# Kernel tuning notes

Hardware: AMD Instinct MI355X
Metric: run time of the kernel (lower is better)

## Reference

```python
import jax, jax.numpy as jnp
import numpy as np
from jax import lax

EPS = 1e-5  # flax BatchNorm default epsilon

def _conv(x, k, b):
    y = lax.conv_general_dilated(x, k, (1, 1), 'SAME', dimension_numbers=('NHWC', 'HWIO', 'NHWC'))
    return y + b

def _bn(x, s, o, m, v):
    # BatchNorm with use_running_average=True (eval mode)
    return (x - m) * (s / jnp.sqrt(v + EPS)) + o

def _pool(x):
    return lax.reduce_window(x, -jnp.inf, lax.max, (1, 2, 2, 1), (1, 2, 2, 1), 'SAME')

def _lstm_last(x_seq, Wi, Wh, b):
    # x_seq: [T,B,D]; Wi: [L,D,4H]; Wh: [L,H,4H]; b: [L,4H].
    # Faithful to original bug: every layer consumes the SAME raw input x_seq
    # (layers are not stacked); only the last layer's hidden states are used.
    B = x_seq.shape[1]
    H = Wh.shape[1]
    def run_layer(Wi_l, Wh_l, b_l):
        def step(carry, xt):
            h, c = carry
            z = xt @ Wi_l + h @ Wh_l + b_l  # [B,4H]
            i, f, g, o = jnp.split(z, 4, axis=-1)
            c2 = jax.nn.sigmoid(f) * c + jax.nn.sigmoid(i) * jnp.tanh(g)
            h2 = jax.nn.sigmoid(o) * jnp.tanh(c2)
            return (h2, c2), h2
        init = (jnp.zeros((B, H), x_seq.dtype), jnp.zeros((B, H), x_seq.dtype))
        _, hs = lax.scan(step, init, x_seq)
        return hs  # [T,B,H]
    hs_all = jax.vmap(run_layer)(Wi, Wh, b)  # [L,T,B,H]
    return hs_all[-1]


def setup_inputs():
    key = jax.random.key(0)
    ks = iter(jax.random.split(key, 64))
    def nrm(shape, scale=0.05):
        return jax.random.normal(next(ks), shape, jnp.float32) * scale
    d = {}
    d['x'] = jax.random.normal(next(ks), (64, 32, 256, 1), jnp.float32)
    cin = [1, 64, 128, 256, 256]
    cout = [64, 128, 256, 256, 512]
    for i in range(5):
        d[f'k{i+1}'] = nrm((3, 3, cin[i], cout[i]))
        d[f'b{i+1}'] = nrm((cout[i],))
        d[f's{i+1}'] = 1.0 + nrm((cout[i],), 0.1)
        d[f'o{i+1}'] = nrm((cout[i],), 0.1)
        d[f'm{i+1}'] = jnp.zeros((cout[i],), jnp.float32)
        d[f'v{i+1}'] = jnp.ones((cout[i],), jnp.float32)
    L, D, H = 2, 2048, 512
    for pre in ('fw', 'bw'):
        d[f'{pre}_Wi'] = nrm((L, D, 4 * H), 0.02)
        d[f'{pre}_Wh'] = nrm((L, H, 4 * H), 0.02)
        d[f'{pre}_b'] = nrm((L, 4 * H), 0.02)
    d['fc_W'] = nrm((2 * H, 80), 0.02)
    d['fc_b'] = nrm((80,), 0.02)
    return d


def reference(x, k1, b1, k2, b2, k3, b3, k4, b4, k5, b5,
              s1, o1, m1, v1, s2, o2, m2, v2, s3, o3, m3, v3,
              s4, o4, m4, v4, s5, o5, m5, v5,
              fw_Wi, fw_Wh, fw_b, bw_Wi, bw_Wh, bw_b, fc_W, fc_b):
    # CNN stem (eval mode: dropout is identity, BN uses running stats)
    x = _pool(_bn(jax.nn.relu(_conv(x, k1, b1)), s1, o1, m1, v1))
    x = _pool(_bn(jax.nn.relu(_conv(x, k2, b2)), s2, o2, m2, v2))
    x = _pool(_bn(jax.nn.relu(_conv(x, k3, b3)), s3, o3, m3, v3))
    x = _bn(jax.nn.relu(_conv(x, k4, b4)), s4, o4, m4, v4)
    x = _bn(jax.nn.relu(_conv(x, k5, b5)), s5, o5, m5, v5)
    b, h, w, c = x.shape
    x = x.reshape(b, w, h * c)        # faithful raw reshape (no transpose), as in original
    x_seq = jnp.swapaxes(x, 0, 1)     # [T,B,D]
    fw = _lstm_last(x_seq, fw_Wi, fw_Wh, fw_b)          # [T,B,H]
    bw = _lstm_last(x_seq[::-1], bw_Wi, bw_Wh, bw_b)    # [T,B,H]; NOT re-flipped (matches original)
    out = jnp.swapaxes(jnp.concatenate([fw, bw], axis=-1), 0, 1)  # [B,T,2H]
    logits = out @ fc_W + fc_b
    return jax.nn.log_softmax(logits, axis=-1)
```

## Files before the change

kernel.cpp:

```cpp
#include <hip/hip_runtime.h>
#include <hip/hip_bf16.h>
#include <math.h>

#define EPSBN 1e-5f

using short8 = __attribute__((ext_vector_type(8))) short;
using f32x4  = __attribute__((ext_vector_type(4))) float;
using us4    = __attribute__((ext_vector_type(4))) unsigned short;

#define MFMA16(a, b, c) __builtin_amdgcn_mfma_f32_16x16x32_bf16(a, b, c, 0, 0, 0)

__device__ __forceinline__ float bf2f(unsigned short u) {
  unsigned int v = ((unsigned int)u) << 16;
  float f;
  __builtin_memcpy(&f, &v, 4);
  return f;
}
__device__ __forceinline__ unsigned short f2bf(float f) {
  __hip_bfloat16 h = __float2bfloat16(f);
  unsigned short u;
  __builtin_memcpy(&u, &h, 2);
  return u;
}
__device__ __forceinline__ float fast_sigmoid(float z) {
  return __builtin_amdgcn_rcpf(1.f + __expf(-z));
}
__device__ __forceinline__ float fast_tanh(float z) {
  float x2 = fminf(fmaxf(2.f * z, -30.f), 30.f);
  float e = __expf(x2);
  return (e - 1.f) * __builtin_amdgcn_rcpf(e + 1.f);
}
__device__ __forceinline__ void stage16(const unsigned short* g, unsigned short* l) {
  __builtin_amdgcn_global_load_lds(
      (const __attribute__((address_space(1))) void*)g,
      (__attribute__((address_space(3))) void*)l, 16, 0, 0);
}

__global__ __launch_bounds__(256) void conv1_pool(
    const float* __restrict__ in, const float* __restrict__ w,
    const float* __restrict__ bias, const float* __restrict__ sc,
    const float* __restrict__ of, const float* __restrict__ mn,
    const float* __restrict__ vr, unsigned short* __restrict__ out) {
  __shared__ float lds[4][258];
  const int blk = blockIdx.x;
  const int b = blk >> 4, y0 = blk & 15;
  const int tid = threadIdx.x;
  for (int i = tid; i < 4 * 258; i += 256) {
    int row = i / 258, c = i - row * 258;
    int iy = 2 * y0 - 1 + row, xx = c - 1;
    float v = 0.f;
    if ((unsigned)iy < 32u && (unsigned)xx < 256u)
      v = in[((b << 5) + iy) * 256 + xx];
    lds[row][c] = v;
  }
  __syncthreads();
  const int co = tid & 63, xg = tid >> 6;
  float w9[9];
  #pragma unroll
  for (int t = 0; t < 9; ++t) w9[t] = w[t * 64 + co];
  const float scale = sc[co] * rsqrtf(vr[co] + EPSBN);
  const float shift = of[co] - mn[co] * scale;
  const float bs = bias[co];
  unsigned short* op = out + (((long)(b * 18 + y0 + 1) * 130 + xg * 32 + 1) << 6) + co;
  for (int px = 0; px < 32; ++px) {
    const int xp = xg * 32 + px;
    float m = -1e30f;
    #pragma unroll
    for (int dy = 0; dy < 2; ++dy) {
      #pragma unroll
      for (int dx = 0; dx < 2; ++dx) {
        const int x = 2 * xp + dx;
        float acc = bs;
        #pragma unroll
        for (int r = 0; r < 3; ++r)
          #pragma unroll
          for (int cc = 0; cc < 3; ++cc)
            acc = fmaf(lds[dy + r][x + cc], w9[r * 3 + cc], acc);
        float v = fmaxf(acc, 0.f) * scale + shift;
        m = fmaxf(m, v);
      }
    }
    op[(long)px << 6] = f2bf(m);
  }
}

template<int C, int H2, int W2>
__global__ __launch_bounds__(256) void maxpool_pad(
    const unsigned short* __restrict__ in, unsigned short* __restrict__ out) {
  constexpr int W2P = W2 + 2, H2P = H2 + 2;
  const int y = blockIdx.y;
  const int b = y / H2P, yp = y - b * H2P;
  const int j = blockIdx.x * 256 + threadIdx.x;
  if (j >= W2P * C) return;
  const int xp = j / C, c = j - xp * C;
  unsigned short res = 0;
  if (yp >= 1 && yp <= H2 && xp >= 1 && xp <= W2) {
    const long rs = (long)(2 * W2) * C;
    const unsigned short* p0 =
        in + (((long)b * (2 * H2) + (yp - 1) * 2) * (2 * W2) + (xp - 1) * 2) * C + c;
    unsigned short u0 = p0[0], u1 = p0[C], u2 = p0[rs], u3 = p0[rs + C];
    unsigned short a = (bf2f(u0) >= bf2f(u1)) ? u0 : u1;
    unsigned short bmx = (bf2f(u2) >= bf2f(u3)) ? u2 : u3;
    res = (bf2f(a) >= bf2f(bmx)) ? a : bmx;
  }
  out[((long)y * W2P + xp) * C + c] = res;
}

struct TAll {
  const float* src[8];
  unsigned short* dst[8];
  int K[8];
  int N[8];
};
__global__ __launch_bounds__(256) void transpose_multi(TAll P) {
  const int z = blockIdx.z;
  const int K = P.K[z], N = P.N[z];
  const int k0 = blockIdx.x * 32, n0 = blockIdx.y * 32;
  if (k0 >= K || n0 >= N) return;
  __shared__ float T[32][33];
  const float* in = P.src[z];
  unsigned short* out = P.dst[z];
  const int tid = threadIdx.x;
  const int r = tid >> 3, c4 = (tid & 7) * 4;
  float4 v = *(const float4*)(in + (long)(k0 + r) * N + n0 + c4);
  T[r][c4 + 0] = v.x; T[r][c4 + 1] = v.y; T[r][c4 + 2] = v.z; T[r][c4 + 3] = v.w;
  __syncthreads();
  us4 o;
  #pragma unroll
  for (int i = 0; i < 4; ++i) o[i] = f2bf(T[c4 + i][r]);
  *(us4*)(out + (long)(n0 + r) * K + k0 + c4) = o;
}

__global__ __launch_bounds__(256) void transpose_fc(
    const float* __restrict__ W, unsigned short* __restrict__ WT) {
  int i = blockIdx.x * 256 + threadIdx.x;
  if (i < 80 * 1024) {
    int n = i >> 10, k = i & 1023;
    WT[i] = f2bf(W[k * 80 + n]);
  }
}

__global__ __launch_bounds__(256) void zero_multi(
    float* p0, long n0, float* p1, long n1, float* p2, long n2, float* p3, long n3) {
  const long i0 = (long)blockIdx.x * 256 + threadIdx.x;
  const long st = (long)gridDim.x * 256;
  for (long j = i0; j < n0; j += st) p0[j] = 0.f;
  for (long j = i0; j < n1; j += st) p1[j] = 0.f;
  for (long j = i0; j < n2; j += st) p2[j] = 0.f;
  for (long j = i0; j < n3; j += st) p3[j] = 0.f;
}

template<int CIN, int COUT, int H, int W, int OUTPAD>
__global__ __launch_bounds__(256) void conv_mfma128(
    const unsigned short* __restrict__ act, const unsigned short* __restrict__ wT,
    const float* __restrict__ bias, const float* __restrict__ sc,
    const float* __restrict__ of, const float* __restrict__ mn,
    const float* __restrict__ vr, unsigned short* __restrict__ out) {
  constexpr int K9 = 9 * CIN;
  constexpr int HW = H * W;
  constexpr int WP = W + 2;
  constexpr int NK = K9 / 32;
  constexpr int CSH = (CIN == 64) ? 1 : (CIN == 128) ? 2 : 3;
  constexpr int CMSK = (1 << CSH) - 1;
  __shared__ unsigned short As[2][4096];
  __shared__ unsigned short Bs[2][4096];
  const int tid = threadIdx.x;
  const int lane = tid & 63, wave = tid >> 6;
  const int m0 = blockIdx.x * 128, n0 = blockIdx.y * 128;
  const int r0 = tid >> 2, seg = tid & 3;
  const int segp = (seg ^ (r0 & 3)) << 3;
  long pa0, pa1;
  {
    const int m = m0 + r0;
    const int b = m / HW, rem = m % HW;
    const int y = rem / W, x = rem % W;
    pa0 = (((long)b * (H + 2) + y) * WP + x) * CIN + segp;
  }
  {
    const int m = m0 + r0 + 64;
    const int b = m / HW, rem = m % HW;
    const int y = rem / W, x = rem % W;
    pa1 = (((long)b * (H + 2) + y) * WP + x) * CIN + segp;
  }
  const long pb0 = (long)(n0 + r0) * K9 + segp;
  const long pb1 = (long)(n0 + r0 + 64) * K9 + segp;
  const int swz = ((lane >> 4) ^ (lane & 3)) << 3;
  const int arow0 = (wave >> 1) * 64 + (lane & 15);
  const int brow0 = (wave & 1) * 64 + (lane & 15);
  f32x4 acc[4][4] = {};

  auto stage_tile = [&](int ks, int buf) {
    const int tap = ks >> CSH;
    const int cib = (ks & CMSK) << 5;
    const int ty = (tap * 86) >> 8;
    const int tx = tap - ty * 3;
    const long ka = (long)(ty * WP + tx) * CIN + cib;
    const long kb = (long)ks << 5;
    unsigned short* aw = &As[buf][wave * 512];
    unsigned short* bw = &Bs[buf][wave * 512];
    stage16(act + pa0 + ka, aw);
    stage16(act + pa1 + ka, aw + 2048);
    stage16(wT + pb0 + kb, bw);
    stage16(wT + pb1 + kb, bw + 2048);
  };

  stage_tile(0, 0);
  #pragma unroll 1
  for (int ks = 0; ks < NK; ++ks) {
    const int buf = ks & 1;
    if (ks + 1 < NK) {
      stage_tile(ks + 1, buf ^ 1);
      asm volatile("s_waitcnt vmcnt(4)" ::: "memory");
    } else {
      asm volatile("s_waitcnt vmcnt(0)" ::: "memory");
    }
    __builtin_amdgcn_s_barrier();
    __builtin_amdgcn_sched_barrier(0);
    short8 a[4], b[4];
    #pragma unroll
    for (int i = 0; i < 4; ++i)
      a[i] = *(const short8*)(&As[buf][(arow0 + i * 16) * 32 + swz]);
    #pragma unroll
    for (int j = 0; j < 4; ++j)
      b[j] = *(const short8*)(&Bs[buf][(brow0 + j * 16) * 32 + swz]);
    #pragma unroll
    for (int i = 0; i < 4; ++i)
      #pragma unroll
      for (int j = 0; j < 4; ++j)
        acc[i][j] = MFMA16(a[i], b[j], acc[i][j]);
    __builtin_amdgcn_s_barrier();
    __builtin_amdgcn_sched_barrier(0);
  }

  float scl[4], shf[4], bsv[4];
  #pragma unroll
  for (int j = 0; j < 4; ++j) {
    const int col = n0 + (wave & 1) * 64 + j * 16 + (lane & 15);
    scl[j] = sc[col] * rsqrtf(vr[col] + EPSBN);
    shf[j] = of[col] - mn[col] * scl[j];
    bsv[j] = bias[col];
  }
  #pragma unroll
  for (int i = 0; i < 4; ++i) {
    #pragma unroll
    for (int rr = 0; rr < 4; ++rr) {
      const int m = m0 + (wave >> 1) * 64 + i * 16 + (lane >> 4) * 4 + rr;
      const int b = m / HW, rem = m % HW;
      const int y = rem / W, x = rem % W;
      long obase;
      if (OUTPAD) obase = (((long)b * (H + 2) + y + 1) * WP + x + 1) * COUT;
      else        obase = (((long)b * H + y) * W + x) * COUT;
      const int colb = n0 + (wave & 1) * 64 + (lane & 15);
      #pragma unroll
      for (int j = 0; j < 4; ++j) {
        const float v = fmaxf(acc[i][j][rr] + bsv[j], 0.f) * scl[j] + shf[j];
        out[obase + colb + j * 16] = f2bf(v);
      }
    }
  }
}

__global__ __launch_bounds__(256) void gemm_xw128(
    const unsigned short* __restrict__ src, const unsigned short* __restrict__ WiT,
    const float* __restrict__ bvec, float* __restrict__ xw, int rev) {
  __shared__ unsigned short As[2][4096];
  __shared__ unsigned short Bs[2][4096];
  const int tid = threadIdx.x;
  const int lane = tid & 63, wave = tid >> 6;
  const int m0 = blockIdx.x * 128, n0 = blockIdx.y * 128;
  const int r0 = tid >> 2, seg = tid & 3;
  const int segp = (seg ^ (r0 & 3)) << 3;
  long pa0, pa1;
  {
    const int r = m0 + r0;
    const int t = r >> 6, bb = r & 63;
    const int tt = rev ? 31 - t : t;
    pa0 = (long)bb * 65536 + (long)tt * 2048 + segp;
  }
  {
    const int r = m0 + r0 + 64;
    const int t = r >> 6, bb = r & 63;
    const int tt = rev ? 31 - t : t;
    pa1 = (long)bb * 65536 + (long)tt * 2048 + segp;
  }
  const long pb0 = (long)(n0 + r0) * 2048 + segp;
  const long pb1 = (long)(n0 + r0 + 64) * 2048 + segp;
  const int swz = ((lane >> 4) ^ (lane & 3)) << 3;
  const int arow0 = (wave >> 1) * 64 + (lane & 15);
  const int brow0 = (wave & 1) * 64 + (lane & 15);
  f32x4 acc[4][4] = {};

  auto stage_tile = [&](int ks, int buf) {
    const long k0 = (long)ks << 5;
    unsigned short* aw = &As[buf][wave * 512];
    unsigned short* bw = &Bs[buf][wave * 512];
    stage16(src + pa0 + k0, aw);
    stage16(src + pa1 + k0, aw + 2048);
    stage16(WiT + pb0 + k0, bw);
    stage16(WiT + pb1 + k0, bw + 2048);
  };

  stage_tile(0, 0);
  #pragma unroll 1
  for (int ks = 0; ks < 64; ++ks) {
    const int buf = ks & 1;
    if (ks + 1 < 64) {
      stage_tile(ks + 1, buf ^ 1);
      asm volatile("s_waitcnt vmcnt(4)" ::: "memory");
    } else {
      asm volatile("s_waitcnt vmcnt(0)" ::: "memory");
    }
    __builtin_amdgcn_s_barrier();
    __builtin_amdgcn_sched_barrier(0);
    short8 a[4], b[4];
    #pragma unroll
    for (int i = 0; i < 4; ++i)
      a[i] = *(const short8*)(&As[buf][(arow0 + i * 16) * 32 + swz]);
    #pragma unroll
    for (int j = 0; j < 4; ++j)
      b[j] = *(const short8*)(&Bs[buf][(brow0 + j * 16) * 32 + swz]);
    #pragma unroll
    for (int i = 0; i < 4; ++i)
      #pragma unroll
      for (int j = 0; j < 4; ++j)
        acc[i][j] = MFMA16(a[i], b[j], acc[i][j]);
    __builtin_amdgcn_s_barrier();
    __builtin_amdgcn_sched_barrier(0);
  }

  float bsv[4];
  #pragma unroll
  for (int j = 0; j < 4; ++j)
    bsv[j] = bvec[n0 + (wave & 1) * 64 + j * 16 + (lane & 15)];
  #pragma unroll
  for (int i = 0; i < 4; ++i) {
    #pragma unroll
    for (int rr = 0; rr < 4; ++rr) {
      const int row = m0 + (wave >> 1) * 64 + i * 16 + (lane >> 4) * 4 + rr;
      const int colb = n0 + (wave & 1) * 64 + (lane & 15);
      #pragma unroll
      for (int j = 0; j < 4; ++j)
        xw[(long)row * 2048 + colb + j * 16] = acc[i][j][rr] + bsv[j];
    }
  }
}

__global__ __launch_bounds__(256) void lstm_persist(
    const unsigned short* __restrict__ WhTF, const unsigned short* __restrict__ WhTB,
    const float* __restrict__ xwF, const float* __restrict__ xwB,
    unsigned short* __restrict__ hsF, unsigned short* __restrict__ hsB,
    int* __restrict__ bar) {
  __shared__ unsigned short Whs[64 * 512];
  __shared__ unsigned short Hs[64 * 512];
  __shared__ float Zs[4 * 64 * 16];
  const int bid = blockIdx.x;
  const int dir = bid >> 5;
  const int nb = bid & 31;
  const int u0 = nb * 16;
  const unsigned short* WhT = dir ? WhTB : WhTF;
  const float* xw = dir ? xwB : xwF;
  unsigned short* hs = dir ? hsB : hsF;
  int* flagbase = bar + dir * 32 * 16;
  int* myflag = flagbase + nb * 16;
  const int tid = threadIdx.x;
  const int lane = tid & 63, wave = tid >> 6;
  const int lr = lane & 15, lk = lane >> 4;
  const int mp = wave >> 1, gp = wave & 1;

  #pragma unroll
  for (int i = 0; i < 16; ++i) {
    const int G = i * 256 + tid;
    const int row = G >> 6, g8 = G & 63;
    const int g = row >> 4, u = row & 15;
    short8 v = *(const short8*)(WhT + ((long)(g * 512 + u0 + u) << 9) + g8 * 8);
    *(short8*)(Whs + row * 512 + ((g8 ^ (row & 7)) << 3)) = v;
  }

  const int prow = tid >> 2;
  const int pu4 = (tid & 3) * 4;
  float c4[4] = {0.f, 0.f, 0.f, 0.f};
  float4 xq[4];
  #pragma unroll
  for (int g = 0; g < 4; ++g)
    xq[g] = *(const float4*)(xw + (long)prow * 2048 + g * 512 + u0 + pu4);

  for (int t = 0; t < 32; ++t) {
    const unsigned short* hsrc = hs + (long)t * 32768;
    #pragma unroll
    for (int i = 0; i < 16; ++i) {
      const int G = i * 256 + tid;
      const int row = G >> 6, g8 = G & 63;
      short8 v = *(const short8*)(hsrc + G * 8);
      *(short8*)(Hs + row * 512 + ((g8 ^ (row & 7)) << 3)) = v;
    }
    __syncthreads();

    f32x4 acc[2][2] = {};
    #pragma unroll
    for (int kk = 0; kk < 16; ++kk) {
      const int sw = ((lk + kk * 4) ^ (lr & 7)) << 3;
      short8 a0 = *(const short8*)(Hs + (mp * 32 + lr) * 512 + sw);
      short8 a1 = *(const short8*)(Hs + (mp * 32 + 16 + lr) * 512 + sw);
      short8 b0 = *(const short8*)(Whs + (gp * 32 + lr) * 512 + sw);
      short8 b1 = *(const short8*)(Whs + (gp * 32 + 16 + lr) * 512 + sw);
      acc[0][0] = MFMA16(a0, b0, acc[0][0]);
      acc[0][1] = MFMA16(a0, b1, acc[0][1]);
      acc[1][0] = MFMA16(a1, b0, acc[1][0]);
      acc[1][1] = MFMA16(a1, b1, acc[1][1]);
    }

    #pragma unroll
    for (int im = 0; im < 2; ++im) {
      const int rowb = (mp * 2 + im) * 16 + lk * 4;
      #pragma unroll
      for (int ig = 0; ig < 2; ++ig) {
        const int g = gp * 2 + ig;
        #pragma unroll
        for (int r = 0; r < 4; ++r)
          Zs[g * 1024 + (rowb + r) * 16 + lr] = acc[im][ig][r];
      }
    }
    __syncthreads();

    {
      float4 zi = *(const float4*)(Zs + tid * 4);
      float4 zf = *(const float4*)(Zs + 1024 + tid * 4);
      float4 zg = *(const float4*)(Zs + 2048 + tid * 4);
      float4 zo = *(const float4*)(Zs + 3072 + tid * 4);
      const float* pzi = (const float*)&zi;
      const float* pzf = (const float*)&zf;
      const float* pzg = (const float*)&zg;
      const float* pzo = (const float*)&zo;
      us4 hv;
      #pragma unroll
      for (int r = 0; r < 4; ++r) {
        float ii = fast_sigmoid(pzi[r] + ((const float*)&xq[0])[r]);
        float ff = fast_sigmoid(pzf[r] + ((const float*)&xq[1])[r]);
        float gg = fast_tanh(pzg[r] + ((const float*)&xq[2])[r]);
        float oo = fast_sigmoid(pzo[r] + ((const float*)&xq[3])[r]);
        c4[r] = ff * c4[r] + ii * gg;
        hv[r] = f2bf(oo * fast_tanh(c4[r]));
      }
      *(us4*)(hs + (long)(t + 1) * 32768 + prow * 512 + u0 + pu4) = hv;
    }

    if (t < 31) {
      float4 xqn[4];
      #pragma unroll
      for (int g = 0; g < 4; ++g)
        xqn[g] = *(const float4*)(xw + (long)((t + 1) * 64 + prow) * 2048 + g * 512 + u0 + pu4);
      __syncthreads();
      if (tid < 64) {
        if (tid == 0)
          __hip_atomic_store(myflag, t + 1, __ATOMIC_RELEASE, __HIP_MEMORY_SCOPE_AGENT);
        int v;
        do {
          v = __hip_atomic_load(flagbase + (tid & 31) * 16,
                                __ATOMIC_ACQUIRE, __HIP_MEMORY_SCOPE_AGENT);
        } while (__any(v < t + 1));
      }
      __syncthreads();
      #pragma unroll
      for (int g = 0; g < 4; ++g) xq[g] = xqn[g];
    }
  }
}

__global__ __launch_bounds__(256) void fc_mfma_ls(
    const unsigned short* __restrict__ hsF, const unsigned short* __restrict__ hsB,
    const unsigned short* __restrict__ WT, const float* __restrict__ bias,
    float* __restrict__ out) {
  __shared__ unsigned short As_[128 * 32];
  __shared__ unsigned short Bs_[80 * 32];
  __shared__ float zbuf[128][81];
  __shared__ float rmax[128];
  __shared__ float rlse[128];
  const int tid = threadIdx.x;
  const int lane = tid & 63, wave = tid >> 6;
  const int m0 = blockIdx.x * 128;
  const int r0 = tid >> 2, seg = tid & 3;
  const int segp = (seg ^ (r0 & 3)) << 3;
  const int swz = ((lane >> 4) ^ (lane & 3)) << 3;
  f32x4 acc[2][5] = {};

  int bA0, tA0, bA1, tA1;
  { int r = m0 + r0;      bA0 = r >> 5; tA0 = r & 31; }
  { int r = m0 + r0 + 64; bA1 = r >> 5; tA1 = r & 31; }

  #pragma unroll 1
  for (int k0 = 0; k0 < 1024; k0 += 32) {
    const unsigned short* src = (k0 < 512) ? hsF : hsB;
    const int koff = k0 & 511;
    stage16(src + (long)(tA0 + 1) * 32768 + bA0 * 512 + koff + segp, As_ + wave * 512);
    stage16(src + (long)(tA1 + 1) * 32768 + bA1 * 512 + koff + segp, As_ + wave * 512 + 2048);
    {
      int G = tid;
      #pragma unroll
      for (int it = 0; it < 2; ++it, G += 256) {
        int rn = G >> 2, sg = G & 3;
        if (rn < 80) {
          short8 v = *(const short8*)(WT + (long)rn * 1024 + k0 + sg * 8);
          *(short8*)(Bs_ + rn * 32 + ((sg ^ (rn & 3)) << 3)) = v;
        }
      }
    }
    __syncthreads();
    short8 a[2], bfrag[5];
    #pragma unroll
    for (int i = 0; i < 2; ++i)
      a[i] = *(const short8*)(As_ + (wave * 32 + i * 16 + (lane & 15)) * 32 + swz);
    #pragma unroll
    for (int j = 0; j < 5; ++j)
      bfrag[j] = *(const short8*)(Bs_ + (j * 16 + (lane & 15)) * 32 + swz);
    #pragma unroll
    for (int i = 0; i < 2; ++i)
      #pragma unroll
      for (int j = 0; j < 5; ++j)
        acc[i][j] = MFMA16(a[i], bfrag[j], acc[i][j]);
    __syncthreads();
  }

  float bsv[5];
  #pragma unroll
  for (int j = 0; j < 5; ++j) bsv[j] = bias[j * 16 + (lane & 15)];
  #pragma unroll
  for (int i = 0; i < 2; ++i)
    #pragma unroll
    for (int j = 0; j < 5; ++j)
      #pragma unroll
      for (int rr = 0; rr < 4; ++rr)
        zbuf[wave * 32 + i * 16 + (lane >> 4) * 4 + rr][j * 16 + (lane & 15)] =
            acc[i][j][rr] + bsv[j];
  __syncthreads();

  if (tid < 128) {
    float mx = -1e30f;
    for (int j = 0; j < 80; ++j) mx = fmaxf(mx, zbuf[tid][j]);
    float s = 0.f;
    for (int j = 0; j < 80; ++j) s += __expf(zbuf[tid][j] - mx);
    rmax[tid] = mx;
    rlse[tid] = logf(s);
  }
  __syncthreads();

  for (int idx = tid; idx < 128 * 80; idx += 256) {
    const int row = idx / 80, j = idx - row * 80;
    out[(long)m0 * 80 + idx] = zbuf[row][j] - rmax[row] - rlse[row];
  }
}

extern "C" void kernel_launch(void* const* d_in, const int* in_sizes, int n_in,
                              void* d_out, int out_size, void* d_ws, size_t ws_size,
                              hipStream_t stream) {
  const float* x  = (const float*)d_in[0];
  const float* k1 = (const float*)d_in[1];  const float* b1 = (const float*)d_in[2];
  const float* s1 = (const float*)d_in[3];  const float* o1 = (const float*)d_in[4];
  const float* m1 = (const float*)d_in[5];  const float* v1 = (const float*)d_in[6];
  const float* k2 = (const float*)d_in[7];  const float* b2 = (const float*)d_in[8];
  const float* s2 = (const float*)d_in[9];  const float* o2 = (const float*)d_in[10];
  const float* m2 = (const float*)d_in[11]; const float* v2 = (const float*)d_in[12];
  const float* k3 = (const float*)d_in[13]; const float* b3 = (const float*)d_in[14];
  const float* s3 = (const float*)d_in[15]; const float* o3 = (const float*)d_in[16];
  const float* m3 = (const float*)d_in[17]; const float* v3 = (const float*)d_in[18];
  const float* k4 = (const float*)d_in[19]; const float* b4 = (const float*)d_in[20];
  const float* s4 = (const float*)d_in[21]; const float* o4 = (const float*)d_in[22];
  const float* m4 = (const float*)d_in[23]; const float* v4 = (const float*)d_in[24];
  const float* k5 = (const float*)d_in[25]; const float* b5 = (const float*)d_in[26];
  const float* s5 = (const float*)d_in[27]; const float* o5 = (const float*)d_in[28];
  const float* m5 = (const float*)d_in[29]; const float* v5 = (const float*)d_in[30];
  const float* fwWi = (const float*)d_in[31];
  const float* fwWh = (const float*)d_in[32];
  const float* fwb  = (const float*)d_in[33];
  const float* bwWi = (const float*)d_in[34];
  const float* bwWh = (const float*)d_in[35];
  const float* bwb  = (const float*)d_in[36];
  const float* fcW  = (const float*)d_in[37];
  const float* fcb  = (const float*)d_in[38];

  char* wsb = (char*)d_ws;
  unsigned short* REG_A = (unsigned short*)(wsb);
  unsigned short* REG_P = (unsigned short*)(wsb + 33554432);
  unsigned short* C4    = (unsigned short*)(wsb + 52723712);
  unsigned short* wT2   = (unsigned short*)(wsb + 59408384);
  unsigned short* wT3   = (unsigned short*)(wsb + 59555840);
  unsigned short* wT4   = (unsigned short*)(wsb + 60145664);
  unsigned short* wT5   = (unsigned short*)(wsb + 61325312);
  unsigned short* WiTF  = (unsigned short*)(wsb + 63684608);
  unsigned short* WiTB  = (unsigned short*)(wsb + 72073216);
  unsigned short* WhTF  = (unsigned short*)(wsb + 80461824);
  unsigned short* WhTB  = (unsigned short*)(wsb + 82558976);
  unsigned short* WTfc  = (unsigned short*)(wsb + 84656128);
  float* xwF = (float*)(wsb + 84819968);
  float* xwB = (float*)(wsb + 101597184);
  int*   bar = (int*)(wsb + 118374400);
  unsigned short* hsF = (unsigned short*)(wsb + 118378496);
  unsigned short* hsB = (unsigned short*)(wsb + 120541184);

  zero_multi<<<2048, 256, 0, stream>>>(
      (float*)(wsb + 118374400), 17408,
      (float*)(wsb + 120541184), 16384,
      (float*)(wsb + 52723712), 1671168,
      (float*)(wsb + 33554432), 4792320);

  TAll tp;
  tp.src[0] = k2; tp.dst[0] = wT2; tp.K[0] = 576;  tp.N[0] = 128;
  tp.src[1] = k3; tp.dst[1] = wT3; tp.K[1] = 1152; tp.N[1] = 256;
  tp.src[2] = k4; tp.dst[2] = wT4; tp.K[2] = 2304; tp.N[2] = 256;
  tp.src[3] = k5; tp.dst[3] = wT5; tp.K[3] = 2304; tp.N[3] = 512;
  tp.src[4] = fwWi + 4194304; tp.dst[4] = WiTF; tp.K[4] = 2048; tp.N[4] = 2048;
  tp.src[5] = bwWi + 4194304; tp.dst[5] = WiTB; tp.K[5] = 2048; tp.N[5] = 2048;
  tp.src[6] = fwWh + 1048576; tp.dst[6] = WhTF; tp.K[6] = 512;  tp.N[6] = 2048;
  tp.src[7] = bwWh + 1048576; tp.dst[7] = WhTB; tp.K[7] = 512;  tp.N[7] = 2048;
  transpose_multi<<<dim3(72, 64, 8), 256, 0, stream>>>(tp);
  transpose_fc<<<320, 256, 0, stream>>>(fcW, WTfc);

  conv1_pool<<<1024, 256, 0, stream>>>(x, k1, b1, s1, o1, m1, v1, REG_P);

  conv_mfma128<64, 128, 16, 128, 0><<<dim3(1024, 1), 256, 0, stream>>>(
      REG_P, wT2, b2, s2, o2, m2, v2, REG_A);
  maxpool_pad<128, 8, 64><<<dim3(33, 640), 256, 0, stream>>>(REG_A, REG_P);

  conv_mfma128<128, 256, 8, 64, 0><<<dim3(256, 2), 256, 0, stream>>>(
      REG_P, wT3, b3, s3, o3, m3, v3, REG_A);
  maxpool_pad<256, 4, 32><<<dim3(34, 384), 256, 0, stream>>>(REG_A, REG_P);

  conv_mfma128<256, 256, 4, 32, 1><<<dim3(64, 2), 256, 0, stream>>>(
      REG_P, wT4, b4, s4, o4, m4, v4, C4);

  conv_mfma128<256, 512, 4, 32, 0><<<dim3(64, 4), 256, 0, stream>>>(
      C4, wT5, b5, s5, o5, m5, v5, REG_A);

  gemm_xw128<<<dim3(16, 16), 256, 0, stream>>>(REG_A, WiTF, fwb + 2048, xwF, 0);
  gemm_xw128<<<dim3(16, 16), 256, 0, stream>>>(REG_A, WiTB, bwb + 2048, xwB, 1);

  lstm_persist<<<64, 256, 0, stream>>>(WhTF, WhTB, xwF, xwB, hsF, hsB, bar);

  fc_mfma_ls<<<16, 256, 0, stream>>>(hsF, hsB, WTfc, fcb, (float*)d_out);
}
```

Before: 499.0 us.

## Merge fw/bw input GEMMs and drop LDS gate shuffle in persistent LSTM

The two input-projection GEMM launches become a single launch, with blockIdx.z selecting the direction. In the persistent LSTM step, each wave now computes all four gates for its own 16 batch rows, so the cell update runs directly from the MFMA accumulators. This removes the Zs LDS round trip and one __syncthreads per step. The flag spin now uses relaxed loads followed by a threadfence, and h is written with nontemporal scalar stores, which are narrower than the previous 4-wide vector writes.

```diff
diff --git a/kernel.cpp b/kernel.cpp
--- a/kernel.cpp
+++ b/kernel.cpp
@@ -260,11 +260,17 @@
   }
 }
 
-__global__ __launch_bounds__(256) void gemm_xw128(
-    const unsigned short* __restrict__ src, const unsigned short* __restrict__ WiT,
-    const float* __restrict__ bvec, float* __restrict__ xw, int rev) {
+__global__ __launch_bounds__(256) void gemm_xw2(
+    const unsigned short* __restrict__ src,
+    const unsigned short* __restrict__ WiTF, const unsigned short* __restrict__ WiTB,
+    const float* __restrict__ bF, const float* __restrict__ bB,
+    float* __restrict__ xwFp, float* __restrict__ xwBp) {
   __shared__ unsigned short As[2][4096];
   __shared__ unsigned short Bs[2][4096];
+  const int rev = blockIdx.z;
+  const unsigned short* WiT = rev ? WiTB : WiTF;
+  const float* bvec = rev ? bB : bF;
+  float* xw = rev ? xwBp : xwFp;
   const int tid = threadIdx.x;
   const int lane = tid & 63, wave = tid >> 6;
   const int m0 = blockIdx.x * 128, n0 = blockIdx.y * 128;
@@ -352,7 +358,6 @@
     int* __restrict__ bar) {
   __shared__ unsigned short Whs[64 * 512];
   __shared__ unsigned short Hs[64 * 512];
-  __shared__ float Zs[4 * 64 * 16];
   const int bid = blockIdx.x;
   const int dir = bid >> 5;
   const int nb = bid & 31;
@@ -365,7 +370,6 @@
   const int tid = threadIdx.x;
   const int lane = tid & 63, wave = tid >> 6;
   const int lr = lane & 15, lk = lane >> 4;
-  const int mp = wave >> 1, gp = wave & 1;
 
   #pragma unroll
   for (int i = 0; i < 16; ++i) {
@@ -376,13 +380,14 @@
     *(short8*)(Whs + row * 512 + ((g8 ^ (row & 7)) << 3)) = v;
   }
 
-  const int prow = tid >> 2;
-  const int pu4 = (tid & 3) * 4;
+  const int myrow0 = wave * 16 + lk * 4;
   float c4[4] = {0.f, 0.f, 0.f, 0.f};
-  float4 xq[4];
+  float xq[4][4];
   #pragma unroll
   for (int g = 0; g < 4; ++g)
-    xq[g] = *(const float4*)(xw + (long)prow * 2048 + g * 512 + u0 + pu4);
+    #pragma unroll
+    for (int r = 0; r < 4; ++r)
+      xq[g][r] = xw[(long)(myrow0 + r) * 2048 + g * 512 + u0 + lr];
 
   for (int t = 0; t < 32; ++t) {
     const unsigned short* hsrc = hs + (long)t * 32768;
@@ -395,73 +400,49 @@
     }
     __syncthreads();
 
-    f32x4 acc[2][2] = {};
+    f32x4 acc[4] = {};
     #pragma unroll
     for (int kk = 0; kk < 16; ++kk) {
       const int sw = ((lk + kk * 4) ^ (lr & 7)) << 3;
-      short8 a0 = *(const short8*)(Hs + (mp * 32 + lr) * 512 + sw);
-      short8 a1 = *(const short8*)(Hs + (mp * 32 + 16 + lr) * 512 + sw);
-      short8 b0 = *(const short8*)(Whs + (gp * 32 + lr) * 512 + sw);
-      short8 b1 = *(const short8*)(Whs + (gp * 32 + 16 + lr) * 512 + sw);
-      acc[0][0] = MFMA16(a0, b0, acc[0][0]);
-      acc[0][1] = MFMA16(a0, b1, acc[0][1]);
-      acc[1][0] = MFMA16(a1, b0, acc[1][0]);
-      acc[1][1] = MFMA16(a1, b1, acc[1][1]);
-    }
-
-    #pragma unroll
-    for (int im = 0; im < 2; ++im) {
-      const int rowb = (mp * 2 + im) * 16 + lk * 4;
-      #pragma unroll
-      for (int ig = 0; ig < 2; ++ig) {
-        const int g = gp * 2 + ig;
+      short8 a = *(const short8*)(Hs + (wave * 16 + lr) * 512 + sw);
+      #pragma unroll
+      for (int g = 0; g < 4; ++g) {
+        short8 b = *(const short8*)(Whs + (g * 16 + lr) * 512 + sw);
+        acc[g] = MFMA16(a, b, acc[g]);
+      }
+    }
+
+    unsigned short* hdst = hs + (long)(t + 1) * 32768;
+    #pragma unroll
+    for (int r = 0; r < 4; ++r) {
+      float ii = fast_sigmoid(acc[0][r] + xq[0][r]);
+      float ff = fast_sigmoid(acc[1][r] + xq[1][r]);
+      float gg = fast_tanh(acc[2][r] + xq[2][r]);
+      float oo = fast_sigmoid(acc[3][r] + xq[3][r]);
+      c4[r] = ff * c4[r] + ii * gg;
+      __builtin_nontemporal_store(
+          f2bf(oo * fast_tanh(c4[r])),
+          hdst + (long)(myrow0 + r) * 512 + u0 + lr);
+    }
+
+    if (t < 31) {
+      #pragma unroll
+      for (int g = 0; g < 4; ++g)
         #pragma unroll
         for (int r = 0; r < 4; ++r)
-          Zs[g * 1024 + (rowb + r) * 16 + lr] = acc[im][ig][r];
-      }
-    }
-    __syncthreads();
-
-    {
-      float4 zi = *(const float4*)(Zs + tid * 4);
-      float4 zf = *(const float4*)(Zs + 1024 + tid * 4);
-      float4 zg = *(const float4*)(Zs + 2048 + tid * 4);
-      float4 zo = *(const float4*)(Zs + 3072 + tid * 4);
-      const float* pzi = (const float*)&zi;
-      const float* pzf = (const float*)&zf;
-      const float* pzg = (const float*)&zg;
-      const float* pzo = (const float*)&zo;
-      us4 hv;
-      #pragma unroll
-      for (int r = 0; r < 4; ++r) {
-        float ii = fast_sigmoid(pzi[r] + ((const float*)&xq[0])[r]);
-        float ff = fast_sigmoid(pzf[r] + ((const float*)&xq[1])[r]);
-        float gg = fast_tanh(pzg[r] + ((const float*)&xq[2])[r]);
-        float oo = fast_sigmoid(pzo[r] + ((const float*)&xq[3])[r]);
-        c4[r] = ff * c4[r] + ii * gg;
-        hv[r] = f2bf(oo * fast_tanh(c4[r]));
-      }
-      *(us4*)(hs + (long)(t + 1) * 32768 + prow * 512 + u0 + pu4) = hv;
-    }
-
-    if (t < 31) {
-      float4 xqn[4];
-      #pragma unroll
-      for (int g = 0; g < 4; ++g)
-        xqn[g] = *(const float4*)(xw + (long)((t + 1) * 64 + prow) * 2048 + g * 512 + u0 + pu4);
+          xq[g][r] = xw[(long)((t + 1) * 64 + myrow0 + r) * 2048 + g * 512 + u0 + lr];
       __syncthreads();
+      if (tid == 0)
+        __hip_atomic_store(myflag, t + 1, __ATOMIC_RELEASE, __HIP_MEMORY_SCOPE_AGENT);
       if (tid < 64) {
-        if (tid == 0)
-          __hip_atomic_store(myflag, t + 1, __ATOMIC_RELEASE, __HIP_MEMORY_SCOPE_AGENT);
         int v;
         do {
           v = __hip_atomic_load(flagbase + (tid & 31) * 16,
-                                __ATOMIC_ACQUIRE, __HIP_MEMORY_SCOPE_AGENT);
+                                __ATOMIC_RELAXED, __HIP_MEMORY_SCOPE_AGENT);
         } while (__any(v < t + 1));
+        __threadfence();
       }
       __syncthreads();
-      #pragma unroll
-      for (int g = 0; g < 4; ++g) xq[g] = xqn[g];
     }
   }
 }
@@ -630,8 +611,8 @@
   conv_mfma128<256, 512, 4, 32, 0><<<dim3(64, 4), 256, 0, stream>>>(
       C4, wT5, b5, s5, o5, m5, v5, REG_A);
 
-  gemm_xw128<<<dim3(16, 16), 256, 0, stream>>>(REG_A, WiTF, fwb + 2048, xwF, 0);
-  gemm_xw128<<<dim3(16, 16), 256, 0, stream>>>(REG_A, WiTB, bwb + 2048, xwB, 1);
+  gemm_xw2<<<dim3(16, 16, 2), 256, 0, stream>>>(
+      REG_A, WiTF, WiTB, fwb + 2048, bwb + 2048, xwF, xwB);
 
   lstm_persist<<<64, 256, 0, stream>>>(WhTF, WhTB, xwF, xwB, hsF, hsB, bar);
 
```

New measurement: 491.0 us. No clear change (-1.6%).
